# Optimization experiments

Hardware: AMD Instinct MI355X
Metric: run time of the kernel (lower is better)

Reference implementation:

```python
import jax, jax.numpy as jnp
import numpy as np

EMB = 768
HEADS = 12
HEAD_DIM = EMB // HEADS
SEQ = 4096
BATCH = 1


def setup_inputs() -> dict:
    key = jax.random.key(0)
    ks = jax.random.split(key, 9)
    s = 1.0 / np.sqrt(EMB)
    return {
        "x": jax.random.normal(ks[0], (BATCH, SEQ, EMB), dtype=jnp.float32),
        "wq": jax.random.normal(ks[1], (EMB, EMB), dtype=jnp.float32) * s,
        "bq": jax.random.normal(ks[2], (EMB,), dtype=jnp.float32) * s,
        "wk": jax.random.normal(ks[3], (EMB, EMB), dtype=jnp.float32) * s,
        "bk": jax.random.normal(ks[4], (EMB,), dtype=jnp.float32) * s,
        "wv": jax.random.normal(ks[5], (EMB, EMB), dtype=jnp.float32) * s,
        "bv": jax.random.normal(ks[6], (EMB,), dtype=jnp.float32) * s,
        "wo": jax.random.normal(ks[7], (EMB, EMB), dtype=jnp.float32) * s,
        "bo": jax.random.normal(ks[8], (EMB,), dtype=jnp.float32) * s,
    }


def reference(x, wq, bq, wk, bk, wv, bv, wo, bo):
    b, n, _ = x.shape
    # projections: [b, n, emb] -> [b, heads, n, head_dim]
    def split_heads(t):
        return t.reshape(b, n, HEADS, HEAD_DIM).transpose(0, 2, 1, 3)
    q = split_heads(x @ wq + bq)
    k = split_heads(x @ wk + bk)
    v = split_heads(x @ wv + bv)
    # full N x N scores (naive attention, as in the original)
    scores = jnp.einsum("bhqd,bhkd->bhqk", q, k)
    causal = jnp.triu(jnp.ones((n, n), dtype=bool), k=1)
    scores = jnp.where(causal, -jnp.inf, scores)
    weights = jax.nn.softmax(scores / np.sqrt(HEAD_DIM), axis=-1)
    # dropout with rate 0.0 is identity (eval mode)
    ctx = jnp.einsum("bhqk,bhkd->bhqd", weights, v)
    ctx = ctx.transpose(0, 2, 1, 3).reshape(b, n, EMB)
    return ctx @ wo + bo
```

## Files before the change

kernel.cpp:

```cpp
#include <hip/hip_runtime.h>
#include <stdint.h>

#define SEQ 4096
#define EMB 768
#define HEADS 12
#define HD 64
#define NQT (SEQ / 64)

typedef __attribute__((ext_vector_type(8))) short short8;
typedef __attribute__((ext_vector_type(4))) short short4v;
typedef __attribute__((ext_vector_type(8))) __bf16 bf16x8;
typedef __attribute__((ext_vector_type(4))) __bf16 bf16x4;
typedef __attribute__((ext_vector_type(4))) float f32x4;

#define QSCALE 0.18033688011112043f

static __device__ __forceinline__ unsigned short f2bf(float f) {
    unsigned int u = __builtin_bit_cast(unsigned int, f);
    unsigned int r = 0x7fffu + ((u >> 16) & 1u);
    u += r;
    return (unsigned short)(u >> 16);
}

static __device__ __forceinline__ f32x4 mfma32(short8 a, short8 b, f32x4 c) {
    return __builtin_amdgcn_mfma_f32_16x16x32_bf16(
        __builtin_bit_cast(bf16x8, a), __builtin_bit_cast(bf16x8, b), c, 0, 0, 0);
}

static __device__ __forceinline__ f32x4 mfma16(short4v a, short4v b, f32x4 c) {
#if __has_builtin(__builtin_amdgcn_mfma_f32_16x16x16_bf16)
    return __builtin_amdgcn_mfma_f32_16x16x16_bf16(
        __builtin_bit_cast(bf16x4, a), __builtin_bit_cast(bf16x4, b), c, 0, 0, 0);
#else
    return __builtin_amdgcn_mfma_f32_16x16x16bf16_1k(a, b, c, 0, 0, 0);
#endif
}

static __device__ __forceinline__ short4v pack4bf(float a, float b, float c, float d) {
#if __has_builtin(__builtin_amdgcn_cvt_pk_bf16_f32)
    typedef __attribute__((ext_vector_type(2))) __bf16 bf16x2;
    bf16x2 lo = __builtin_amdgcn_cvt_pk_bf16_f32(a, b);
    bf16x2 hi = __builtin_amdgcn_cvt_pk_bf16_f32(c, d);
    uint2 u = {__builtin_bit_cast(unsigned int, lo), __builtin_bit_cast(unsigned int, hi)};
    return __builtin_bit_cast(short4v, u);
#else
    short4v p;
    p[0] = (short)f2bf(a); p[1] = (short)f2bf(b);
    p[2] = (short)f2bf(c); p[3] = (short)f2bf(d);
    return p;
#endif
}

static __device__ __forceinline__ void load_lds16(const void* g, void* l) {
    __builtin_amdgcn_global_load_lds(
        (const __attribute__((address_space(1))) unsigned int*)(uintptr_t)g,
        (__attribute__((address_space(3))) unsigned int*)(uintptr_t)l, 16, 0, 0);
}

static __device__ __forceinline__ int pid_of(int h, int qt, int ch) {
    int b = (qt < 40) ? (qt - 20) : (qt < 60 ? 20 + (qt - 40) * 2 : 60 + (qt - 60) * 3);
    return h * 72 + b + (ch - 1);
}

__global__ __launch_bounds__(256) void convert_all(const float* __restrict__ x,
                                                   const float* __restrict__ wq,
                                                   const float* __restrict__ wk,
                                                   const float* __restrict__ wv,
                                                   const float* __restrict__ wo,
                                                   unsigned short* __restrict__ xb,
                                                   unsigned short* __restrict__ wqkvT,
                                                   unsigned short* __restrict__ woT) {
    __shared__ float Ls[64][65];
    const int bid = blockIdx.x;
    if (bid < 3072) {
        int i = bid * 256 + threadIdx.x;
        float4 v = ((const float4*)x)[i];
        ushort4 o = {f2bf(v.x), f2bf(v.y), f2bf(v.z), f2bf(v.w)};
        ((ushort4*)xb)[i] = o;
        return;
    }
    const int idx = bid - 3072;
    const int z = idx / 144;
    const int bx = (idx % 144) / 12, by = idx % 12;
    const float* W = (z == 0) ? wq : (z == 1) ? wk : (z == 2) ? wv : wo;
    unsigned short* dst = (z < 3) ? (wqkvT + (size_t)z * EMB * EMB) : woT;
    const int k0 = bx * 64, n0 = by * 64;
    const int r = threadIdx.x >> 2, c0 = (threadIdx.x & 3) * 16;
    for (int j = 0; j < 16; j += 4) {
        float4 v = *(const float4*)&W[(size_t)(k0 + r) * EMB + n0 + c0 + j];
        Ls[r][c0 + j] = v.x;
        Ls[r][c0 + j + 1] = v.y;
        Ls[r][c0 + j + 2] = v.z;
        Ls[r][c0 + j + 3] = v.w;
    }
    __syncthreads();
    unsigned short tmp[16];
    for (int j = 0; j < 16; j++) tmp[j] = f2bf(Ls[c0 + j][r]);
    *(uint4*)&dst[(size_t)(n0 + r) * EMB + k0 + c0] = *(uint4*)tmp;
    *(uint4*)&dst[(size_t)(n0 + r) * EMB + k0 + c0 + 8] = *(uint4*)(tmp + 8);
}

__global__ __launch_bounds__(256) void gemm_qkv(const unsigned short* __restrict__ A,
                                                const unsigned short* __restrict__ Bt,
                                                const float* __restrict__ b0p,
                                                const float* __restrict__ b1p,
                                                const float* __restrict__ b2p,
                                                unsigned short* __restrict__ QKb,
                                                unsigned short* __restrict__ Vtb) {
    __shared__ __align__(16) unsigned short SMEM[8192];
    unsigned short* As = SMEM;
    unsigned short* Bs = SMEM + 4096;
    const int tid = threadIdx.x;
    const int wave = tid >> 6, lane = tid & 63, quad = lane >> 4, l16 = lane & 15;
    const int m0 = blockIdx.x * 128, n0 = blockIdx.y * 128;
    const int wm = (wave >> 1) * 64, wn = (wave & 1) * 64;
    const int lrow = lane >> 2, lcol = (lane & 3) * 8;

    f32x4 acc[4][4] = {};

    for (int k0 = 0; k0 < EMB; k0 += 32) {
        __syncthreads();
        for (int t = 0; t < 2; t++) {
            int row = wave * 32 + t * 16 + lrow;
            load_lds16(&A[(size_t)(m0 + row) * EMB + k0 + lcol], &As[(wave * 2 + t) * 512]);
            load_lds16(&Bt[(size_t)(n0 + row) * EMB + k0 + lcol], &Bs[(wave * 2 + t) * 512]);
        }
        __syncthreads();
        short8 a[4], b[4];
        for (int i = 0; i < 4; i++) a[i] = *(const short8*)&As[(wm + i * 16 + l16) * 32 + quad * 8];
        for (int i = 0; i < 4; i++) b[i] = *(const short8*)&Bs[(wn + i * 16 + l16) * 32 + quad * 8];
        for (int i = 0; i < 4; i++)
            for (int j = 0; j < 4; j++) acc[i][j] = mfma32(a[i], b[j], acc[i][j]);
    }

    const int z = n0 / EMB;
    if (z < 2) {
        const float* bias = z ? b1p : b0p;
        const float sc = z ? 1.0f : QSCALE;
        for (int i = 0; i < 4; i++)
            for (int j = 0; j < 4; j++) {
                int mbase = m0 + wm + i * 16 + quad * 4;
                int n = n0 + wn + j * 16 + l16;
                float bv = bias[n - z * EMB];
                for (int r = 0; r < 4; r++)
                    QKb[(size_t)(mbase + r) * 1536 + n] = f2bf((acc[i][j][r] + bv) * sc);
            }
    } else {
        const int nn = n0 + wn + l16 - 2 * EMB;
        for (int j = 0; j < 4; j++) {
            __syncthreads();
            const float bv = b2p[nn + j * 16];
            const int nloc = (wave & 1) * 16 + l16;
            for (int i = 0; i < 4; i++) {
                ushort4 pk;
                pk.x = f2bf(acc[i][j][0] + bv);
                pk.y = f2bf(acc[i][j][1] + bv);
                pk.z = f2bf(acc[i][j][2] + bv);
                pk.w = f2bf(acc[i][j][3] + bv);
                *(ushort4*)&SMEM[nloc * 136 + wm + i * 16 + quad * 4] = pk;
            }
            __syncthreads();
            const int nl = tid >> 3, c = tid & 7;
            const int ng = (nl >> 4) * 64 + j * 16 + (nl & 15) + n0 + 0 * 0 - 2 * EMB;
            const int hh = ng >> 6, dd = ng & 63;
            unsigned short* dst = &Vtb[(size_t)(hh * HD + dd) * SEQ + m0];
            *(uint4*)&dst[c * 8] = *(uint4*)&SMEM[nl * 136 + c * 8];
            *(uint4*)&dst[64 + c * 8] = *(uint4*)&SMEM[nl * 136 + 64 + c * 8];
        }
    }
}

__global__ __launch_bounds__(256) void gemm_out(const unsigned short* __restrict__ A,
                                                const unsigned short* __restrict__ Bt,
                                                const float* __restrict__ bias,
                                                float* __restrict__ outp) {
    __shared__ __align__(16) unsigned short As[64 * 32];
    __shared__ __align__(16) unsigned short Bs[128 * 32];
    const int tid = threadIdx.x;
    const int wave = tid >> 6, lane = tid & 63, quad = lane >> 4, l16 = lane & 15;
    const int m0 = blockIdx.x * 64, n0 = blockIdx.y * 128;
    const int wm = (wave >> 1) * 32, wn = (wave & 1) * 64;
    const int lrow = lane >> 2, lcol = (lane & 3) * 8;

    f32x4 acc[2][4] = {};

    for (int k0 = 0; k0 < EMB; k0 += 32) {
        __syncthreads();
        load_lds16(&A[(size_t)(m0 + wave * 16 + lrow) * EMB + k0 + lcol], &As[wave * 512]);
        for (int t = 0; t < 2; t++) {
            int row = wave * 32 + t * 16 + lrow;
            load_lds16(&Bt[(size_t)(n0 + row) * EMB + k0 + lcol], &Bs[(wave * 2 + t) * 512]);
        }
        __syncthreads();
        short8 a[2], b[4];
        for (int i = 0; i < 2; i++) a[i] = *(const short8*)&As[(wm + i * 16 + l16) * 32 + quad * 8];
        for (int j = 0; j < 4; j++) b[j] = *(const short8*)&Bs[(wn + j * 16 + l16) * 32 + quad * 8];
        for (int i = 0; i < 2; i++)
            for (int j = 0; j < 4; j++) acc[i][j] = mfma32(a[i], b[j], acc[i][j]);
    }

    for (int i = 0; i < 2; i++)
        for (int j = 0; j < 4; j++) {
            int mbase = m0 + wm + i * 16 + quad * 4;
            int n = n0 + wn + j * 16 + l16;
            float bv = bias[n];
            for (int r = 0; r < 4; r++) outp[(size_t)(mbase + r) * EMB + n] = acc[i][j][r] + bv;
        }
}

__global__ __launch_bounds__(256) void attn_kernel(const unsigned short* __restrict__ QKb,
                                                   const unsigned short* __restrict__ Vtb,
                                                   unsigned short* __restrict__ ctxb,
                                                   unsigned short* __restrict__ Op,
                                                   float* __restrict__ mArr,
                                                   float* __restrict__ lArr) {
    __shared__ __align__(16) unsigned short Ks[64 * 64];
    __shared__ __align__(16) unsigned short Vs[64 * 64];

    const int bid = blockIdx.x;
    const int h = bid % HEADS;
    const int rem = 135 - bid / HEADS;
    int qt, ch, nch;
    if (rem < 20) {
        qt = rem; ch = 0; nch = 1;
    } else if (rem < 60) {
        int t = rem - 20; qt = 20 + (t >> 1); ch = t & 1; nch = 2;
    } else if (rem < 120) {
        int t = rem - 60; qt = 40 + t / 3; ch = t % 3; nch = 3;
    } else {
        int t = rem - 120; qt = 60 + (t >> 2); ch = t & 3; nch = 4;
    }
    const int kb = ch * (qt + 1) / nch;
    const int ke = (ch + 1) * (qt + 1) / nch - 1;
    const int qbase = qt * 64;
    const int tid = threadIdx.x;
    const int wave = tid >> 6, lane = tid & 63, quad = lane >> 4, l16 = lane & 15;

    const unsigned short* Qg = QKb + (size_t)h * HD;
    const unsigned short* Kg = QKb + (size_t)(EMB + h * HD);
    const unsigned short* Vh = Vtb + (size_t)h * HD * SEQ;

    const int q = qbase + wave * 16 + l16;
    const short8 bQ0 = *(const short8*)&Qg[(size_t)q * 1536 + quad * 8];
    const short8 bQ1 = *(const short8*)&Qg[(size_t)q * 1536 + 32 + quad * 8];

    const int row = tid >> 2, t4 = tid & 3, cg = t4 * 16;
    const int swk = row & 7, swv = row & 15;

    f32x4 O[4] = {};
    float m_i = -3.0e38f, l_i = 0.f;

    uint4 kr0, kr1, vr0, vr1;
    {
        const int kb64 = kb * 64;
        kr0 = *(const uint4*)&Kg[(size_t)(kb64 + row) * 1536 + cg];
        kr1 = *(const uint4*)&Kg[(size_t)(kb64 + row) * 1536 + cg + 8];
        vr0 = *(const uint4*)&Vh[(size_t)row * SEQ + kb64 + cg];
        vr1 = *(const uint4*)&Vh[(size_t)row * SEQ + kb64 + cg + 8];
    }

    for (int kt = kb; kt <= ke; kt++) {
        const int kbase = kt * 64;
        __syncthreads();
        *(uint4*)&Ks[row * 64 + ((2 * t4) ^ swk) * 8] = kr0;
        *(uint4*)&Ks[row * 64 + ((2 * t4 + 1) ^ swk) * 8] = kr1;
        *(uint2*)&Vs[row * 64 + ((4 * t4) ^ swv) * 4] = ((const uint2*)&vr0)[0];
        *(uint2*)&Vs[row * 64 + ((4 * t4 + 1) ^ swv) * 4] = ((const uint2*)&vr0)[1];
        *(uint2*)&Vs[row * 64 + ((4 * t4 + 2) ^ swv) * 4] = ((const uint2*)&vr1)[0];
        *(uint2*)&Vs[row * 64 + ((4 * t4 + 3) ^ swv) * 4] = ((const uint2*)&vr1)[1];
        if (kt < ke) {
            const int nb = kbase + 64;
            kr0 = *(const uint4*)&Kg[(size_t)(nb + row) * 1536 + cg];
            kr1 = *(const uint4*)&Kg[(size_t)(nb + row) * 1536 + cg + 8];
            vr0 = *(const uint4*)&Vh[(size_t)row * SEQ + nb + cg];
            vr1 = *(const uint4*)&Vh[(size_t)row * SEQ + nb + cg + 8];
        }
        __syncthreads();

        const int swr = l16 & 7;
        f32x4 st[4];
        for (int nt = 0; nt < 4; nt++) {
            short8 aK0 = *(const short8*)&Ks[(nt * 16 + l16) * 64 + (quad ^ swr) * 8];
            short8 aK1 = *(const short8*)&Ks[(nt * 16 + l16) * 64 + ((quad + 4) ^ swr) * 8];
            f32x4 z = {};
            z = mfma32(aK0, bQ0, z);
            z = mfma32(aK1, bQ1, z);
            st[nt] = z;
        }
        if (kt == qt) {
            for (int nt = 0; nt < 4; nt++)
                for (int r = 0; r < 4; r++)
                    if (kbase + nt * 16 + quad * 4 + r > q) st[nt][r] = -INFINITY;
        }
        float mx = -3.0e38f;
        for (int nt = 0; nt < 4; nt++)
            for (int r = 0; r < 4; r++) mx = fmaxf(mx, st[nt][r]);
        mx = fmaxf(mx, __shfl_xor(mx, 16));
        mx = fmaxf(mx, __shfl_xor(mx, 32));
        const bool inc = mx > m_i;
        if (__ballot(inc)) {
            const float mn = inc ? mx : m_i;
            const float alpha = __builtin_amdgcn_exp2f(m_i - mn);
            m_i = mn;
            l_i *= alpha;
            for (int dt = 0; dt < 4; dt++)
                for (int r = 0; r < 4; r++) O[dt][r] *= alpha;
        }
        float rs = 0.f;
        short4v pk[4];
        for (int nt = 0; nt < 4; nt++) {
            float p0 = __builtin_amdgcn_exp2f(st[nt][0] - m_i);
            float p1 = __builtin_amdgcn_exp2f(st[nt][1] - m_i);
            float p2 = __builtin_amdgcn_exp2f(st[nt][2] - m_i);
            float p3 = __builtin_amdgcn_exp2f(st[nt][3] - m_i);
            rs += p0 + p1 + p2 + p3;
            pk[nt] = pack4bf(p0, p1, p2, p3);
        }
        rs += __shfl_xor(rs, 16);
        rs += __shfl_xor(rs, 32);
        l_i += rs;
        for (int dt = 0; dt < 4; dt++)
            for (int nt = 0; nt < 4; nt++) {
                short4v av = *(const short4v*)&Vs[(dt * 16 + l16) * 64 + ((4 * nt + quad) ^ l16) * 4];
                O[dt] = mfma16(av, pk[nt], O[dt]);
            }
    }

    const int ql = wave * 16 + l16;
    if (nch == 1) {
        const float inv = 1.f / l_i;
        for (int dt = 0; dt < 4; dt++) {
            ushort4 o;
            o.x = f2bf(O[dt][0] * inv);
            o.y = f2bf(O[dt][1] * inv);
            o.z = f2bf(O[dt][2] * inv);
            o.w = f2bf(O[dt][3] * inv);
            *(ushort4*)&ctxb[(size_t)q * EMB + h * HD + dt * 16 + quad * 4] = o;
        }
    } else {
        if (ch == 0) {
            for (int dt = 0; dt < 4; dt++) {
                ushort4 o;
                o.x = f2bf(O[dt][0]);
                o.y = f2bf(O[dt][1]);
                o.z = f2bf(O[dt][2]);
                o.w = f2bf(O[dt][3]);
                *(ushort4*)&ctxb[(size_t)q * EMB + h * HD + dt * 16 + quad * 4] = o;
            }
        } else {
            const int pid = pid_of(h, qt, ch);
            for (int dt = 0; dt < 4; dt++) {
                ushort4 o;
                o.x = f2bf(O[dt][0]);
                o.y = f2bf(O[dt][1]);
                o.z = f2bf(O[dt][2]);
                o.w = f2bf(O[dt][3]);
                *(ushort4*)&Op[(size_t)pid * 4096 + ql * 64 + dt * 16 + quad * 4] = o;
            }
        }
        if (quad == 0) {
            const int mli = ((h * 64 + qt) * 4 + ch) * 64 + ql;
            mArr[mli] = m_i;
            lArr[mli] = l_i;
        }
    }
}

__global__ __launch_bounds__(256) void merge_kernel(const unsigned short* __restrict__ Op,
                                                    const float* __restrict__ mArr,
                                                    const float* __restrict__ lArr,
                                                    unsigned short* __restrict__ ctxb) {
    const int gid = blockIdx.x;
    const int h = gid / 44;
    const int qt = 20 + gid % 44;
    const int nch = (qt < 40) ? 2 : (qt < 60) ? 3 : 4;
    const int q = threadIdx.x >> 2, d0 = (threadIdx.x & 3) * 16;
    const int mlbase = (h * 64 + qt) * 4;

    float mc[4], lc[4];
    for (int c = 0; c < nch; c++) {
        mc[c] = mArr[(mlbase + c) * 64 + q];
        lc[c] = lArr[(mlbase + c) * 64 + q];
    }
    float M = mc[0];
    for (int c = 1; c < nch; c++) M = fmaxf(M, mc[c]);
    float w[4], L = 0.f;
    for (int c = 0; c < nch; c++) {
        w[c] = __builtin_amdgcn_exp2f(mc[c] - M);
        L += w[c] * lc[c];
    }
    const float inv = 1.f / L;
    for (int c = 0; c < nch; c++) w[c] *= inv;

    unsigned short* dst = &ctxb[(size_t)(qt * 64 + q) * EMB + h * HD + d0];
    for (int jj = 0; jj < 16; jj += 8) {
        uint4 u0 = *(const uint4*)&dst[jj];
        float f[8];
        const unsigned short* p0 = (const unsigned short*)&u0;
        for (int t = 0; t < 8; t++)
            f[t] = w[0] * __builtin_bit_cast(float, (unsigned int)p0[t] << 16);
        for (int c = 1; c < nch; c++) {
            const int pid = pid_of(h, qt, c);
            uint4 u = *(const uint4*)&Op[(size_t)pid * 4096 + q * 64 + d0 + jj];
            const unsigned short* p = (const unsigned short*)&u;
            for (int t = 0; t < 8; t++)
                f[t] += w[c] * __builtin_bit_cast(float, (unsigned int)p[t] << 16);
        }
        unsigned short o[8];
        for (int t = 0; t < 8; t++) o[t] = f2bf(f[t]);
        *(uint4*)&dst[jj] = *(uint4*)o;
    }
}

extern "C" void kernel_launch(void* const* d_in, const int* in_sizes, int n_in,
                              void* d_out, int out_size, void* d_ws, size_t ws_size,
                              hipStream_t stream) {
    const float* x = (const float*)d_in[0];
    const float* wq = (const float*)d_in[1];
    const float* bq = (const float*)d_in[2];
    const float* wk = (const float*)d_in[3];
    const float* bk = (const float*)d_in[4];
    const float* wv = (const float*)d_in[5];
    const float* bv = (const float*)d_in[6];
    const float* wo = (const float*)d_in[7];
    const float* bo = (const float*)d_in[8];

    unsigned short* ws = (unsigned short*)d_ws;
    unsigned short* xb = ws;
    unsigned short* wqkvT = xb + SEQ * EMB;
    unsigned short* woT = wqkvT + 3 * EMB * EMB;
    unsigned short* QKb = woT + EMB * EMB;
    unsigned short* Vtb = QKb + (size_t)SEQ * 1536;
    unsigned short* ctxb = Vtb + HEADS * SEQ * HD;
    unsigned short* Op = xb;
    float* mArr = (float*)(ws + 864 * 4096);
    float* lArr = mArr + 12 * 64 * 4 * 64;

    convert_all<<<dim3(3072 + 576), 256, 0, stream>>>(x, wq, wk, wv, wo, xb, wqkvT, woT);
    gemm_qkv<<<dim3(SEQ / 128, 3 * EMB / 128), 256, 0, stream>>>(
        xb, wqkvT, bq, bk, bv, QKb, Vtb);
    attn_kernel<<<dim3(12 * 136), 256, 0, stream>>>(QKb, Vtb, ctxb, Op, mArr, lArr);
    merge_kernel<<<dim3(528), 256, 0, stream>>>(Op, mArr, lArr, ctxb);
    gemm_out<<<dim3(SEQ / 64, EMB / 128), 256, 0, stream>>>(ctxb, woT, bo, (float*)d_out);
}
```

Measured before the change: 205.3 us.

## Process 128 query rows per attention block to reuse K/V tiles across two groups

The attention kernel now handles two 64-row query groups per block, so each K/V tile loaded into LDS feeds twice as much MFMA work. The work split and the merge kernel are rebuilt around 128-row query tiles with a new chunk schedule and partial-buffer layout, and the first group is skipped on fully masked tiles. The QK projection epilogue is also restaged through LDS so global stores are coalesced. This roughly halves K/V traffic and block count, at the cost of higher register pressure (launch bounds now 4) and fewer blocks available for load balancing.

```diff
diff --git a/kernel.cpp b/kernel.cpp
--- a/kernel.cpp
+++ b/kernel.cpp
@@ -5,7 +5,6 @@
 #define EMB 768
 #define HEADS 12
 #define HD 64
-#define NQT (SEQ / 64)
 
 typedef __attribute__((ext_vector_type(8))) short short8;
 typedef __attribute__((ext_vector_type(4))) short short4v;
@@ -57,9 +56,40 @@
         (__attribute__((address_space(3))) unsigned int*)(uintptr_t)l, 16, 0, 0);
 }
 
-static __device__ __forceinline__ int pid_of(int h, int qt, int ch) {
-    int b = (qt < 40) ? (qt - 20) : (qt < 60 ? 20 + (qt - 40) * 2 : 60 + (qt - 60) * 3);
-    return h * 72 + b + (ch - 1);
+static __device__ __forceinline__ int pid_of(int h, int i128, int ch) {
+    int b = (i128 < 18) ? (i128 - 9)
+                        : (i128 < 27 ? 9 + (i128 - 18) * 2 : 27 + (i128 - 27) * 3);
+    return h * 42 + b + (ch - 1);
+}
+
+static __device__ __forceinline__ void softmax_step(f32x4* st, float& m_i, float& l_i,
+                                                    f32x4* O, short4v* pk) {
+    float mx = -3.0e38f;
+    for (int nt = 0; nt < 4; nt++)
+        for (int r = 0; r < 4; r++) mx = fmaxf(mx, st[nt][r]);
+    mx = fmaxf(mx, __shfl_xor(mx, 16));
+    mx = fmaxf(mx, __shfl_xor(mx, 32));
+    const bool inc = mx > m_i;
+    if (__ballot(inc)) {
+        const float mn = inc ? mx : m_i;
+        const float alpha = __builtin_amdgcn_exp2f(m_i - mn);
+        m_i = mn;
+        l_i *= alpha;
+        for (int dt = 0; dt < 4; dt++)
+            for (int r = 0; r < 4; r++) O[dt][r] *= alpha;
+    }
+    float rs = 0.f;
+    for (int nt = 0; nt < 4; nt++) {
+        float p0 = __builtin_amdgcn_exp2f(st[nt][0] - m_i);
+        float p1 = __builtin_amdgcn_exp2f(st[nt][1] - m_i);
+        float p2 = __builtin_amdgcn_exp2f(st[nt][2] - m_i);
+        float p3 = __builtin_amdgcn_exp2f(st[nt][3] - m_i);
+        rs += p0 + p1 + p2 + p3;
+        pk[nt] = pack4bf(p0, p1, p2, p3);
+    }
+    rs += __shfl_xor(rs, 16);
+    rs += __shfl_xor(rs, 32);
+    l_i += rs;
 }
 
 __global__ __launch_bounds__(256) void convert_all(const float* __restrict__ x,
@@ -107,7 +137,7 @@
                                                 const float* __restrict__ b2p,
                                                 unsigned short* __restrict__ QKb,
                                                 unsigned short* __restrict__ Vtb) {
-    __shared__ __align__(16) unsigned short SMEM[8192];
+    __shared__ __align__(16) unsigned short SMEM[64 * 136];
     unsigned short* As = SMEM;
     unsigned short* Bs = SMEM + 4096;
     const int tid = threadIdx.x;
@@ -137,14 +167,23 @@
     if (z < 2) {
         const float* bias = z ? b1p : b0p;
         const float sc = z ? 1.0f : QSCALE;
-        for (int i = 0; i < 4; i++)
-            for (int j = 0; j < 4; j++) {
-                int mbase = m0 + wm + i * 16 + quad * 4;
-                int n = n0 + wn + j * 16 + l16;
-                float bv = bias[n - z * EMB];
-                for (int r = 0; r < 4; r++)
-                    QKb[(size_t)(mbase + r) * 1536 + n] = f2bf((acc[i][j][r] + bv) * sc);
-            }
+        float bv[4];
+        for (int j = 0; j < 4; j++) bv[j] = bias[n0 + wn + j * 16 + l16 - z * EMB];
+        for (int half = 0; half < 2; half++) {
+            __syncthreads();
+            if ((wave >> 1) == half) {
+                for (int i = 0; i < 4; i++)
+                    for (int j = 0; j < 4; j++)
+                        for (int r = 0; r < 4; r++)
+                            SMEM[(i * 16 + quad * 4 + r) * 136 + wn + j * 16 + l16] =
+                                f2bf((acc[i][j][r] + bv[j]) * sc);
+            }
+            __syncthreads();
+            const int row = tid >> 2, seg = tid & 3;
+            unsigned short* dst = &QKb[(size_t)(m0 + half * 64 + row) * 1536 + n0 + seg * 32];
+            for (int u = 0; u < 4; u++)
+                *(uint4*)&dst[u * 8] = *(uint4*)&SMEM[row * 136 + seg * 32 + u * 8];
+        }
     } else {
         const int nn = n0 + wn + l16 - 2 * EMB;
         for (int j = 0; j < 4; j++) {
@@ -161,7 +200,7 @@
             }
             __syncthreads();
             const int nl = tid >> 3, c = tid & 7;
-            const int ng = (nl >> 4) * 64 + j * 16 + (nl & 15) + n0 + 0 * 0 - 2 * EMB;
+            const int ng = (nl >> 4) * 64 + j * 16 + (nl & 15) + n0 - 2 * EMB;
             const int hh = ng >> 6, dd = ng & 63;
             unsigned short* dst = &Vtb[(size_t)(hh * HD + dd) * SEQ + m0];
             *(uint4*)&dst[c * 8] = *(uint4*)&SMEM[nl * 136 + c * 8];
@@ -208,31 +247,32 @@
         }
 }
 
-__global__ __launch_bounds__(256) void attn_kernel(const unsigned short* __restrict__ QKb,
-                                                   const unsigned short* __restrict__ Vtb,
-                                                   unsigned short* __restrict__ ctxb,
-                                                   unsigned short* __restrict__ Op,
-                                                   float* __restrict__ mArr,
-                                                   float* __restrict__ lArr) {
+__global__ __launch_bounds__(256, 4) void attn_kernel(const unsigned short* __restrict__ QKb,
+                                                      const unsigned short* __restrict__ Vtb,
+                                                      unsigned short* __restrict__ ctxb,
+                                                      unsigned short* __restrict__ Op,
+                                                      float* __restrict__ mArr,
+                                                      float* __restrict__ lArr) {
     __shared__ __align__(16) unsigned short Ks[64 * 64];
     __shared__ __align__(16) unsigned short Vs[64 * 64];
 
     const int bid = blockIdx.x;
     const int h = bid % HEADS;
-    const int rem = 135 - bid / HEADS;
-    int qt, ch, nch;
-    if (rem < 20) {
-        qt = rem; ch = 0; nch = 1;
-    } else if (rem < 60) {
-        int t = rem - 20; qt = 20 + (t >> 1); ch = t & 1; nch = 2;
-    } else if (rem < 120) {
-        int t = rem - 60; qt = 40 + t / 3; ch = t % 3; nch = 3;
+    const int r2 = 73 - bid / HEADS;
+    int i128, ch, nch;
+    if (r2 < 9) {
+        i128 = r2; ch = 0; nch = 1;
+    } else if (r2 < 27) {
+        int t = r2 - 9; i128 = 9 + (t >> 1); ch = t & 1; nch = 2;
+    } else if (r2 < 54) {
+        int t = r2 - 27; i128 = 18 + t / 3; ch = t % 3; nch = 3;
     } else {
-        int t = rem - 120; qt = 60 + (t >> 2); ch = t & 3; nch = 4;
-    }
-    const int kb = ch * (qt + 1) / nch;
-    const int ke = (ch + 1) * (qt + 1) / nch - 1;
-    const int qbase = qt * 64;
+        int t = r2 - 54; i128 = 27 + (t >> 2); ch = t & 3; nch = 4;
+    }
+    const int T = 2 * i128 + 2;
+    const int kb = ch * T / nch;
+    const int ke = (ch + 1) * T / nch - 1;
+    const int qbase = i128 * 128;
     const int tid = threadIdx.x;
     const int wave = tid >> 6, lane = tid & 63, quad = lane >> 4, l16 = lane & 15;
 
@@ -240,15 +280,18 @@
     const unsigned short* Kg = QKb + (size_t)(EMB + h * HD);
     const unsigned short* Vh = Vtb + (size_t)h * HD * SEQ;
 
-    const int q = qbase + wave * 16 + l16;
-    const short8 bQ0 = *(const short8*)&Qg[(size_t)q * 1536 + quad * 8];
-    const short8 bQ1 = *(const short8*)&Qg[(size_t)q * 1536 + 32 + quad * 8];
+    const int q0 = qbase + wave * 16 + l16;
+    const int q1 = q0 + 64;
+    const short8 bQ00 = *(const short8*)&Qg[(size_t)q0 * 1536 + quad * 8];
+    const short8 bQ01 = *(const short8*)&Qg[(size_t)q0 * 1536 + 32 + quad * 8];
+    const short8 bQ10 = *(const short8*)&Qg[(size_t)q1 * 1536 + quad * 8];
+    const short8 bQ11 = *(const short8*)&Qg[(size_t)q1 * 1536 + 32 + quad * 8];
 
     const int row = tid >> 2, t4 = tid & 3, cg = t4 * 16;
     const int swk = row & 7, swv = row & 15;
 
-    f32x4 O[4] = {};
-    float m_i = -3.0e38f, l_i = 0.f;
+    f32x4 O0[4] = {}, O1[4] = {};
+    float m0i = -3.0e38f, l0i = 0.f, m1i = -3.0e38f, l1i = 0.f;
 
     uint4 kr0, kr1, vr0, vr1;
     {
@@ -277,91 +320,99 @@
         }
         __syncthreads();
 
+        const bool g0act = (kbase <= qbase + wave * 16 + 15);
+
         const int swr = l16 & 7;
-        f32x4 st[4];
+        f32x4 st0[4], st1[4];
         for (int nt = 0; nt < 4; nt++) {
             short8 aK0 = *(const short8*)&Ks[(nt * 16 + l16) * 64 + (quad ^ swr) * 8];
             short8 aK1 = *(const short8*)&Ks[(nt * 16 + l16) * 64 + ((quad + 4) ^ swr) * 8];
-            f32x4 z = {};
-            z = mfma32(aK0, bQ0, z);
-            z = mfma32(aK1, bQ1, z);
-            st[nt] = z;
-        }
-        if (kt == qt) {
+            f32x4 z1 = {};
+            z1 = mfma32(aK0, bQ10, z1);
+            z1 = mfma32(aK1, bQ11, z1);
+            st1[nt] = z1;
+            if (g0act) {
+                f32x4 z0 = {};
+                z0 = mfma32(aK0, bQ00, z0);
+                z0 = mfma32(aK1, bQ01, z0);
+                st0[nt] = z0;
+            }
+        }
+        if (g0act && kbase + 63 > qbase + wave * 16) {
             for (int nt = 0; nt < 4; nt++)
                 for (int r = 0; r < 4; r++)
-                    if (kbase + nt * 16 + quad * 4 + r > q) st[nt][r] = -INFINITY;
-        }
-        float mx = -3.0e38f;
-        for (int nt = 0; nt < 4; nt++)
-            for (int r = 0; r < 4; r++) mx = fmaxf(mx, st[nt][r]);
-        mx = fmaxf(mx, __shfl_xor(mx, 16));
-        mx = fmaxf(mx, __shfl_xor(mx, 32));
-        const bool inc = mx > m_i;
-        if (__ballot(inc)) {
-            const float mn = inc ? mx : m_i;
-            const float alpha = __builtin_amdgcn_exp2f(m_i - mn);
-            m_i = mn;
-            l_i *= alpha;
+                    if (kbase + nt * 16 + quad * 4 + r > q0) st0[nt][r] = -INFINITY;
+        }
+        if (kbase + 63 > qbase + 64 + wave * 16) {
+            for (int nt = 0; nt < 4; nt++)
+                for (int r = 0; r < 4; r++)
+                    if (kbase + nt * 16 + quad * 4 + r > q1) st1[nt][r] = -INFINITY;
+        }
+
+        short4v pk0[4], pk1[4];
+        softmax_step(st1, m1i, l1i, O1, pk1);
+        if (g0act) softmax_step(st0, m0i, l0i, O0, pk0);
+
+        if (g0act) {
             for (int dt = 0; dt < 4; dt++)
-                for (int r = 0; r < 4; r++) O[dt][r] *= alpha;
-        }
-        float rs = 0.f;
-        short4v pk[4];
-        for (int nt = 0; nt < 4; nt++) {
-            float p0 = __builtin_amdgcn_exp2f(st[nt][0] - m_i);
-            float p1 = __builtin_amdgcn_exp2f(st[nt][1] - m_i);
-            float p2 = __builtin_amdgcn_exp2f(st[nt][2] - m_i);
-            float p3 = __builtin_amdgcn_exp2f(st[nt][3] - m_i);
-            rs += p0 + p1 + p2 + p3;
-            pk[nt] = pack4bf(p0, p1, p2, p3);
-        }
-        rs += __shfl_xor(rs, 16);
-        rs += __shfl_xor(rs, 32);
-        l_i += rs;
-        for (int dt = 0; dt < 4; dt++)
-            for (int nt = 0; nt < 4; nt++) {
-                short4v av = *(const short4v*)&Vs[(dt * 16 + l16) * 64 + ((4 * nt + quad) ^ l16) * 4];
-                O[dt] = mfma16(av, pk[nt], O[dt]);
-            }
-    }
-
-    const int ql = wave * 16 + l16;
-    if (nch == 1) {
-        const float inv = 1.f / l_i;
-        for (int dt = 0; dt < 4; dt++) {
-            ushort4 o;
-            o.x = f2bf(O[dt][0] * inv);
-            o.y = f2bf(O[dt][1] * inv);
-            o.z = f2bf(O[dt][2] * inv);
-            o.w = f2bf(O[dt][3] * inv);
-            *(ushort4*)&ctxb[(size_t)q * EMB + h * HD + dt * 16 + quad * 4] = o;
-        }
-    } else {
-        if (ch == 0) {
+                for (int nt = 0; nt < 4; nt++) {
+                    short4v av =
+                        *(const short4v*)&Vs[(dt * 16 + l16) * 64 + ((4 * nt + quad) ^ l16) * 4];
+                    O1[dt] = mfma16(av, pk1[nt], O1[dt]);
+                    O0[dt] = mfma16(av, pk0[nt], O0[dt]);
+                }
+        } else {
+            for (int dt = 0; dt < 4; dt++)
+                for (int nt = 0; nt < 4; nt++) {
+                    short4v av =
+                        *(const short4v*)&Vs[(dt * 16 + l16) * 64 + ((4 * nt + quad) ^ l16) * 4];
+                    O1[dt] = mfma16(av, pk1[nt], O1[dt]);
+                }
+        }
+    }
+
+    for (int g = 0; g < 2; g++) {
+        f32x4* O = g ? O1 : O0;
+        const float mi = g ? m1i : m0i;
+        const float li = g ? l1i : l0i;
+        const int qglob = g ? q1 : q0;
+        const int ql = g * 64 + wave * 16 + l16;
+        if (nch == 1) {
+            const float inv = 1.f / li;
             for (int dt = 0; dt < 4; dt++) {
                 ushort4 o;
-                o.x = f2bf(O[dt][0]);
-                o.y = f2bf(O[dt][1]);
-                o.z = f2bf(O[dt][2]);
-                o.w = f2bf(O[dt][3]);
-                *(ushort4*)&ctxb[(size_t)q * EMB + h * HD + dt * 16 + quad * 4] = o;
+                o.x = f2bf(O[dt][0] * inv);
+                o.y = f2bf(O[dt][1] * inv);
+                o.z = f2bf(O[dt][2] * inv);
+                o.w = f2bf(O[dt][3] * inv);
+                *(ushort4*)&ctxb[(size_t)qglob * EMB + h * HD + dt * 16 + quad * 4] = o;
             }
         } else {
-            const int pid = pid_of(h, qt, ch);
-            for (int dt = 0; dt < 4; dt++) {
-                ushort4 o;
-                o.x = f2bf(O[dt][0]);
-                o.y = f2bf(O[dt][1]);
-                o.z = f2bf(O[dt][2]);
-                o.w = f2bf(O[dt][3]);
-                *(ushort4*)&Op[(size_t)pid * 4096 + ql * 64 + dt * 16 + quad * 4] = o;
-            }
-        }
-        if (quad == 0) {
-            const int mli = ((h * 64 + qt) * 4 + ch) * 64 + ql;
-            mArr[mli] = m_i;
-            lArr[mli] = l_i;
+            if (ch == 0) {
+                for (int dt = 0; dt < 4; dt++) {
+                    ushort4 o;
+                    o.x = f2bf(O[dt][0]);
+                    o.y = f2bf(O[dt][1]);
+                    o.z = f2bf(O[dt][2]);
+                    o.w = f2bf(O[dt][3]);
+                    *(ushort4*)&ctxb[(size_t)qglob * EMB + h * HD + dt * 16 + quad * 4] = o;
+                }
+            } else {
+                const int pid = pid_of(h, i128, ch);
+                for (int dt = 0; dt < 4; dt++) {
+                    ushort4 o;
+                    o.x = f2bf(O[dt][0]);
+                    o.y = f2bf(O[dt][1]);
+                    o.z = f2bf(O[dt][2]);
+                    o.w = f2bf(O[dt][3]);
+                    *(ushort4*)&Op[(size_t)pid * 8192 + ql * 64 + dt * 16 + quad * 4] = o;
+                }
+            }
+            if (quad == 0) {
+                const int mli = ((h * 32 + i128) * 4 + ch) * 128 + ql;
+                mArr[mli] = mi;
+                lArr[mli] = li;
+            }
         }
     }
 }
@@ -371,16 +422,16 @@
                                                     const float* __restrict__ lArr,
                                                     unsigned short* __restrict__ ctxb) {
     const int gid = blockIdx.x;
-    const int h = gid / 44;
-    const int qt = 20 + gid % 44;
-    const int nch = (qt < 40) ? 2 : (qt < 60) ? 3 : 4;
-    const int q = threadIdx.x >> 2, d0 = (threadIdx.x & 3) * 16;
-    const int mlbase = (h * 64 + qt) * 4;
+    const int h = gid % HEADS;
+    const int i128 = 9 + gid / HEADS;
+    const int nch = (i128 < 18) ? 2 : (i128 < 27) ? 3 : 4;
+    const int q = threadIdx.x >> 1, d0 = (threadIdx.x & 1) * 32;
+    const int mlbase = (h * 32 + i128) * 4;
 
     float mc[4], lc[4];
     for (int c = 0; c < nch; c++) {
-        mc[c] = mArr[(mlbase + c) * 64 + q];
-        lc[c] = lArr[(mlbase + c) * 64 + q];
+        mc[c] = mArr[(mlbase + c) * 128 + q];
+        lc[c] = lArr[(mlbase + c) * 128 + q];
     }
     float M = mc[0];
     for (int c = 1; c < nch; c++) M = fmaxf(M, mc[c]);
@@ -392,16 +443,16 @@
     const float inv = 1.f / L;
     for (int c = 0; c < nch; c++) w[c] *= inv;
 
-    unsigned short* dst = &ctxb[(size_t)(qt * 64 + q) * EMB + h * HD + d0];
-    for (int jj = 0; jj < 16; jj += 8) {
+    unsigned short* dst = &ctxb[(size_t)(i128 * 128 + q) * EMB + h * HD + d0];
+    for (int jj = 0; jj < 32; jj += 8) {
         uint4 u0 = *(const uint4*)&dst[jj];
         float f[8];
         const unsigned short* p0 = (const unsigned short*)&u0;
         for (int t = 0; t < 8; t++)
             f[t] = w[0] * __builtin_bit_cast(float, (unsigned int)p0[t] << 16);
         for (int c = 1; c < nch; c++) {
-            const int pid = pid_of(h, qt, c);
-            uint4 u = *(const uint4*)&Op[(size_t)pid * 4096 + q * 64 + d0 + jj];
+            const int pid = pid_of(h, i128, c);
+            uint4 u = *(const uint4*)&Op[(size_t)pid * 8192 + q * 64 + d0 + jj];
             const unsigned short* p = (const unsigned short*)&u;
             for (int t = 0; t < 8; t++)
                 f[t] += w[c] * __builtin_bit_cast(float, (unsigned int)p[t] << 16);
@@ -433,13 +484,13 @@
     unsigned short* Vtb = QKb + (size_t)SEQ * 1536;
     unsigned short* ctxb = Vtb + HEADS * SEQ * HD;
     unsigned short* Op = xb;
-    float* mArr = (float*)(ws + 864 * 4096);
-    float* lArr = mArr + 12 * 64 * 4 * 64;
+    float* mArr = (float*)(ws + 4128768);
+    float* lArr = (float*)(ws + 4521984);
 
     convert_all<<<dim3(3072 + 576), 256, 0, stream>>>(x, wq, wk, wv, wo, xb, wqkvT, woT);
     gemm_qkv<<<dim3(SEQ / 128, 3 * EMB / 128), 256, 0, stream>>>(
         xb, wqkvT, bq, bk, bv, QKb, Vtb);
-    attn_kernel<<<dim3(12 * 136), 256, 0, stream>>>(QKb, Vtb, ctxb, Op, mArr, lArr);
-    merge_kernel<<<dim3(528), 256, 0, stream>>>(Op, mArr, lArr, ctxb);
+    attn_kernel<<<dim3(12 * 74), 256, 0, stream>>>(QKb, Vtb, ctxb, Op, mArr, lArr);
+    merge_kernel<<<dim3(276), 256, 0, stream>>>(Op, mArr, lArr, ctxb);
     gemm_out<<<dim3(SEQ / 64, EMB / 128), 256, 0, stream>>>(ctxb, woT, bo, (float*)d_out);
 }
```

Measured after the change: 226.9 us. 1.11x slower.
